# Kernel tuning notes

Hardware: AMD Instinct MI355X
Metric: run time of the kernel (lower is better)

## Reference

```python
import jax, jax.numpy as jnp
import numpy as np
import math

D_K = 64
DROP_P = 0.5

def setup_inputs() -> dict:
    key = jax.random.key(0)
    kq, kk, kv, km = jax.random.split(key, 4)
    B, S, d = 32, 2048, D_K
    Q = jax.random.normal(kq, (B, S, d), dtype=jnp.float32)
    K = jax.random.normal(kk, (B, S, d), dtype=jnp.float32)
    V = jax.random.normal(kv, (B, S, d), dtype=jnp.float32)
    # Bernoulli(keep_prob) mask for training-mode dropout (p=0.5)
    dropout_mask = jax.random.bernoulli(km, 1.0 - DROP_P, (B, S, S))
    return {"Q": Q, "K": K, "V": V, "dropout_mask": dropout_mask}

def reference(Q, K, V, dropout_mask):
    # attn = softmax(Q K^T / sqrt(d_k)); dropout; y = attn V
    scale = 1.0 / math.sqrt(D_K)
    scores = jnp.einsum('bqd,bkd->bqk', Q, K) * scale   # [B,S,S]
    attn = jax.nn.softmax(scores, axis=-1)
    keep_scale = 1.0 / (1.0 - DROP_P)
    attn = jnp.where(dropout_mask, attn * keep_scale, 0.0)
    y = jnp.einsum('bqk,bkd->bqd', attn, V)             # [B,S,d]
    return (y, attn)
```

## Files before the change

kernel.cpp:

```cpp
#include <hip/hip_runtime.h>
#include <hip/hip_bf16.h>
#include <stdint.h>

#define SQ 2048
#define DK 64
#define NB 32
#define TQ 16
#define EW 2064
#define NTHREADS 512
#define SCL 0.18033688011112042f

typedef __attribute__((ext_vector_type(8))) short short8;
typedef __attribute__((ext_vector_type(4))) float f32x4;
typedef __attribute__((ext_vector_type(4))) unsigned u32x4;
typedef __attribute__((ext_vector_type(2))) unsigned u32x2;

__device__ __forceinline__ unsigned f2bf_u(float x) {
    unsigned u = __builtin_bit_cast(unsigned, x);
    u += 0x7fffu + ((u >> 16) & 1u);
    return u >> 16;
}
__device__ __forceinline__ float bf2f(unsigned h) {
    return __builtin_bit_cast(float, h << 16);
}
__device__ __forceinline__ void split8(const float* p, short8& h, short8& l) {
    f32x4 a = *(const f32x4*)p;
    f32x4 b = *(const f32x4*)(p + 4);
    #pragma unroll
    for (int j = 0; j < 4; ++j) {
        unsigned ua = f2bf_u(a[j]);
        h[j] = (short)ua; l[j] = (short)f2bf_u(a[j] - bf2f(ua));
        unsigned ub = f2bf_u(b[j]);
        h[j + 4] = (short)ub; l[j + 4] = (short)f2bf_u(b[j] - bf2f(ub));
    }
}
__device__ __forceinline__ unsigned pkf16(float a, float b) {
    unsigned short ha = __builtin_bit_cast(unsigned short, (_Float16)a);
    unsigned short hb = __builtin_bit_cast(unsigned short, (_Float16)b);
    return (unsigned)ha | ((unsigned)hb << 16);
}
__device__ __forceinline__ float upk16(unsigned u, int hi) {
    return (float)__builtin_bit_cast(_Float16, (unsigned short)(hi ? (u >> 16) : (u & 0xffffu)));
}

__global__ __launch_bounds__(256) void prep_kernel(
    const float* __restrict__ K, const float* __restrict__ V,
    unsigned short* __restrict__ Khi, unsigned short* __restrict__ Klo,
    unsigned short* __restrict__ Vt)
{
    __shared__ float vtile[64][65];
    const int t  = threadIdx.x;
    const int b  = blockIdx.x >> 5;
    const int s0 = (blockIdx.x & 31) << 6;
    const size_t base = ((size_t)b * SQ + s0) * DK + (size_t)t * 16;

    {
        short8 h0, l0, h1, l1;
        split8(K + base,     h0, l0);
        split8(K + base + 8, h1, l1);
        *(short8*)(Khi + base)     = h0;
        *(short8*)(Khi + base + 8) = h1;
        *(short8*)(Klo + base)     = l0;
        *(short8*)(Klo + base + 8) = l1;
    }
    {
        const int sr = t >> 2, dc = (t & 3) << 4;
        #pragma unroll
        for (int u = 0; u < 16; u += 4) {
            f32x4 v = *(const f32x4*)(V + base + u);
            vtile[sr][dc + u + 0] = v[0];
            vtile[sr][dc + u + 1] = v[1];
            vtile[sr][dc + u + 2] = v[2];
            vtile[sr][dc + u + 3] = v[3];
        }
    }
    __syncthreads();
    #pragma unroll
    for (int rep = 0; rep < 16; ++rep) {
        const int idx = rep * 256 + t;
        const int d = idx >> 6, s = idx & 63;
        Vt[((size_t)b * DK + d) * SQ + s0 + s] = (unsigned short)f2bf_u(vtile[s][d]);
    }
}

__global__ __launch_bounds__(NTHREADS, 4) void sdpa_main(
    const float* __restrict__ Q, const unsigned short* __restrict__ Khi,
    const unsigned short* __restrict__ Klo, const unsigned short* __restrict__ Vt,
    const unsigned* __restrict__ Mk, float* __restrict__ Yout, float* __restrict__ Aout)
{
    __shared__ __align__(16) unsigned short e_lds[TQ][EW];
    __shared__ float yp[4][TQ][16];
    __shared__ float rsum[8][TQ];
    __shared__ float i2s[TQ];

    const int tid  = threadIdx.x;
    const int lane = tid & 63;
    const int wv   = tid >> 6;
    const int m16  = lane & 15;
    const int kq   = lane >> 4;
    const int koff = kq * 8;

    const int b  = blockIdx.x >> 7;
    const int q0 = (blockIdx.x & 127) * TQ;

    const int cr = tid >> 5;
    const int cc = (tid & 31) * 8;
    const int xc = (cr & 7) << 3;
    const size_t crow = ((size_t)b * SQ + q0 + cr) * SQ + cc;

    u32x4 ma0 = __builtin_nontemporal_load((const u32x4*)(Mk + crow));
    u32x4 mb0 = __builtin_nontemporal_load((const u32x4*)(Mk + crow + 4));
    u32x4 ma1 = __builtin_nontemporal_load((const u32x4*)(Mk + crow + 256));
    u32x4 mb1 = __builtin_nontemporal_load((const u32x4*)(Mk + crow + 256 + 4));

    short8 qh[2], ql[2];
    {
        const float* qrow = Q + ((size_t)b * SQ + q0 + m16) * DK;
        split8(qrow + koff,      qh[0], ql[0]);
        split8(qrow + 32 + koff, qh[1], ql[1]);
    }

    float rs = 0.f;
    {
        const size_t krow = ((size_t)b * SQ + wv * 256 + m16) * DK;
        const unsigned short* khp = Khi + krow;
        const unsigned short* klp = Klo + krow;
        const int xw = (m16 & 7) << 3;
        for (int t = 0; t < 16; ++t) {
            const int off = t * 16 * DK;
            f32x4 acc = {0.f, 0.f, 0.f, 0.f};
            #pragma unroll
            for (int c = 0; c < 2; ++c) {
                short8 kh = *(const short8*)(khp + off + c * 32 + koff);
                short8 kl = *(const short8*)(klp + off + c * 32 + koff);
                acc = __builtin_amdgcn_mfma_f32_16x16x32_bf16(kh, qh[c], acc, 0, 0, 0);
                acc = __builtin_amdgcn_mfma_f32_16x16x32_bf16(kh, ql[c], acc, 0, 0, 0);
                acc = __builtin_amdgcn_mfma_f32_16x16x32_bf16(kl, qh[c], acc, 0, 0, 0);
            }
            const float e0 = exp2f(acc[0] * SCL);
            const float e1 = exp2f(acc[1] * SCL);
            const float e2 = exp2f(acc[2] * SCL);
            const float e3 = exp2f(acc[3] * SCL);
            rs += (e0 + e1) + (e2 + e3);
            u32x2 pk;
            pk[0] = pkf16(e0, e1);
            pk[1] = pkf16(e2, e3);
            *(u32x2*)&e_lds[m16][(wv * 256 + t * 16 + kq * 4) ^ xw] = pk;
        }
    }
    rs += __shfl_xor(rs, 16);
    rs += __shfl_xor(rs, 32);
    if (lane < 16) rsum[wv][lane] = rs;
    __syncthreads();
    if (tid < 16) {
        float s = 0.f;
        #pragma unroll
        for (int w = 0; w < 8; ++w) s += rsum[w][tid];
        i2s[tid] = 2.0f / s;
    }
    __syncthreads();

    const float i2 = i2s[cr];

    const int g   = wv >> 1;
    const int par = wv & 1;
    const int xm  = (m16 & 7) << 3;
    const unsigned short* vrow = Vt + ((size_t)b * DK + g * 16 + m16) * SQ;
    f32x4 acc = {0.f, 0.f, 0.f, 0.f};

    #define C_FINISH(s, ma, mb)                                                   \
    {                                                                             \
        unsigned short* ep = &e_lds[cr][((s) * 256 + cc) ^ xc];                   \
        const u32x4 ev = *(const u32x4*)ep;                                       \
        const float a0 = (ma)[0] ? upk16(ev[0], 0) * i2 : 0.f;                    \
        const float a1 = (ma)[1] ? upk16(ev[0], 1) * i2 : 0.f;                    \
        const float a2 = (ma)[2] ? upk16(ev[1], 0) * i2 : 0.f;                    \
        const float a3 = (ma)[3] ? upk16(ev[1], 1) * i2 : 0.f;                    \
        const float a4 = (mb)[0] ? upk16(ev[2], 0) * i2 : 0.f;                    \
        const float a5 = (mb)[1] ? upk16(ev[2], 1) * i2 : 0.f;                    \
        const float a6 = (mb)[2] ? upk16(ev[3], 0) * i2 : 0.f;                    \
        const float a7 = (mb)[3] ? upk16(ev[3], 1) * i2 : 0.f;                    \
        f32x4 av0 = {a0, a1, a2, a3};                                             \
        f32x4 av1 = {a4, a5, a6, a7};                                             \
        __builtin_nontemporal_store(av0, (f32x4*)(Aout + crow + (s) * 256));      \
        __builtin_nontemporal_store(av1, (f32x4*)(Aout + crow + (s) * 256 + 4));  \
        u32x4 pb;                                                                 \
        pb[0] = f2bf_u(a0) | (f2bf_u(a1) << 16);                                  \
        pb[1] = f2bf_u(a2) | (f2bf_u(a3) << 16);                                  \
        pb[2] = f2bf_u(a4) | (f2bf_u(a5) << 16);                                  \
        pb[3] = f2bf_u(a6) | (f2bf_u(a7) << 16);                                  \
        *(u32x4*)ep = pb;                                                         \
    }

    #define PV_STRIPE(s)                                                          \
    {                                                                             \
        _Pragma("unroll")                                                         \
        for (int c = 0; c < 4; ++c) {                                             \
            const int k0 = (s) * 256 + par * 128 + c * 32;                        \
            short8 af = *(const short8*)&e_lds[m16][(k0 + koff) ^ xm];            \
            short8 vf = *(const short8*)(vrow + k0 + koff);                       \
            acc = __builtin_amdgcn_mfma_f32_16x16x32_bf16(af, vf, acc, 0, 0, 0);  \
        }                                                                         \
    }

    #define CBAR()                                                                \
        asm volatile("s_waitcnt lgkmcnt(0)" ::: "memory");                        \
        __builtin_amdgcn_s_barrier();                                             \
        __builtin_amdgcn_sched_barrier(0);

    #define REFILL(slotA, slotB, s)                                               \
        slotA = __builtin_nontemporal_load((const u32x4*)(Mk + crow + (s) * 256));\
        slotB = __builtin_nontemporal_load((const u32x4*)(Mk + crow + (s) * 256 + 4));

    C_FINISH(0, ma0, mb0);
    CBAR();

    REFILL(ma0, mb0, 2); PV_STRIPE(0); C_FINISH(1, ma1, mb1); CBAR();
    REFILL(ma1, mb1, 3); PV_STRIPE(1); C_FINISH(2, ma0, mb0); CBAR();
    REFILL(ma0, mb0, 4); PV_STRIPE(2); C_FINISH(3, ma1, mb1); CBAR();
    REFILL(ma1, mb1, 5); PV_STRIPE(3); C_FINISH(4, ma0, mb0); CBAR();
    REFILL(ma0, mb0, 6); PV_STRIPE(4); C_FINISH(5, ma1, mb1); CBAR();
    REFILL(ma1, mb1, 7); PV_STRIPE(5); C_FINISH(6, ma0, mb0); CBAR();
                         PV_STRIPE(6); C_FINISH(7, ma1, mb1); CBAR();
                         PV_STRIPE(7);

    #undef REFILL
    #undef CBAR
    #undef PV_STRIPE
    #undef C_FINISH

    if (par == 1) {
        #pragma unroll
        for (int r = 0; r < 4; ++r) yp[g][kq * 4 + r][m16] = acc[r];
    }
    __syncthreads();
    if (par == 0) {
        #pragma unroll
        for (int r = 0; r < 4; ++r) {
            const float yv = acc[r] + yp[g][kq * 4 + r][m16];
            __builtin_nontemporal_store(yv,
                Yout + ((size_t)b * SQ + q0 + kq * 4 + r) * DK + g * 16 + m16);
        }
    }
}

extern "C" void kernel_launch(void* const* d_in, const int* in_sizes, int n_in,
                              void* d_out, int out_size, void* d_ws, size_t ws_size,
                              hipStream_t stream) {
    const float*    Q  = (const float*)d_in[0];
    const float*    K  = (const float*)d_in[1];
    const float*    V  = (const float*)d_in[2];
    const unsigned* Mk = (const unsigned*)d_in[3];
    float* Yout = (float*)d_out;
    float* Aout = (float*)d_out + (size_t)NB * SQ * DK;

    const size_t NEL = (size_t)NB * SQ * DK;
    unsigned short* Khi = (unsigned short*)d_ws;
    unsigned short* Klo = Khi + NEL;
    unsigned short* Vt  = Klo + NEL;

    prep_kernel<<<dim3(NB * (SQ / 64)), dim3(256), 0, stream>>>(K, V, Khi, Klo, Vt);
    sdpa_main<<<dim3(NB * (SQ / TQ)), dim3(NTHREADS), 0, stream>>>(
        Q, Khi, Klo, Vt, Mk, Yout, Aout);
}
```

Baseline: 499.2 us.

## Apply dropout mask in QK phase and defer normalization to output

Moves the dropout mask application into the QK^T/exp phase, storing masked unnormalized exponentials as bf16 in LDS. The PV matmul now consumes these directly without a per-stripe rewrite pass or barriers, and the 1/sum scale is applied once to Y at the end and to A when it is written. This removes the LDS read-modify-write and the barrier chain between the C and PV stripes. In exchange, attention output values are now rounded to bf16 before scaling, which loses precision compared with the previous fp16 path, and the mask loads move into the compute loop.

```diff
diff --git a/kernel.cpp b/kernel.cpp
--- a/kernel.cpp
+++ b/kernel.cpp
@@ -22,6 +22,9 @@
 }
 __device__ __forceinline__ float bf2f(unsigned h) {
     return __builtin_bit_cast(float, h << 16);
+}
+__device__ __forceinline__ float bf2f_hi(unsigned u) {
+    return __builtin_bit_cast(float, u & 0xffff0000u);
 }
 __device__ __forceinline__ void split8(const float* p, short8& h, short8& l) {
     f32x4 a = *(const f32x4*)p;
@@ -33,14 +36,6 @@
         unsigned ub = f2bf_u(b[j]);
         h[j + 4] = (short)ub; l[j + 4] = (short)f2bf_u(b[j] - bf2f(ub));
     }
-}
-__device__ __forceinline__ unsigned pkf16(float a, float b) {
-    unsigned short ha = __builtin_bit_cast(unsigned short, (_Float16)a);
-    unsigned short hb = __builtin_bit_cast(unsigned short, (_Float16)b);
-    return (unsigned)ha | ((unsigned)hb << 16);
-}
-__device__ __forceinline__ float upk16(unsigned u, int hi) {
-    return (float)__builtin_bit_cast(_Float16, (unsigned short)(hi ? (u >> 16) : (u & 0xffffu)));
 }
 
 __global__ __launch_bounds__(256) void prep_kernel(
@@ -103,64 +98,80 @@
     const int b  = blockIdx.x >> 7;
     const int q0 = (blockIdx.x & 127) * TQ;
 
+    short8 qh[2], ql[2];
+    {
+        const float* qrow = Q + ((size_t)b * SQ + q0 + m16) * DK;
+        split8(qrow + koff,      qh[0], ql[0]);
+        split8(qrow + 32 + koff, qh[1], ql[1]);
+    }
+
+    float rs = 0.f;
+    {
+        const size_t krow = ((size_t)b * SQ + wv * 256 + m16) * DK;
+        const unsigned short* khp = Khi + krow;
+        const unsigned short* klp = Klo + krow;
+        const unsigned* mrow = Mk + ((size_t)b * SQ + q0 + m16) * SQ + wv * 256 + kq * 4;
+        const int xw = (m16 & 7) << 3;
+
+        u32x4 m0, m1, m2, m3, m4, m5, m6, m7;
+
+        #define LOADM(dst, t) dst = *(const u32x4*)(mrow + (t) * 16);
+        #define AITER(t, M)                                                           \
+        {                                                                             \
+            const int off = (t) * 16 * DK;                                            \
+            f32x4 acc = {0.f, 0.f, 0.f, 0.f};                                         \
+            _Pragma("unroll")                                                         \
+            for (int c = 0; c < 2; ++c) {                                             \
+                short8 kh = *(const short8*)(khp + off + c * 32 + koff);              \
+                short8 kl = *(const short8*)(klp + off + c * 32 + koff);              \
+                acc = __builtin_amdgcn_mfma_f32_16x16x32_bf16(kh, qh[c], acc, 0, 0, 0);\
+                acc = __builtin_amdgcn_mfma_f32_16x16x32_bf16(kh, ql[c], acc, 0, 0, 0);\
+                acc = __builtin_amdgcn_mfma_f32_16x16x32_bf16(kl, qh[c], acc, 0, 0, 0);\
+            }                                                                         \
+            const float e0 = exp2f(acc[0] * SCL);                                     \
+            const float e1 = exp2f(acc[1] * SCL);                                     \
+            const float e2 = exp2f(acc[2] * SCL);                                     \
+            const float e3 = exp2f(acc[3] * SCL);                                     \
+            rs += (e0 + e1) + (e2 + e3);                                              \
+            const float a0 = (M)[0] ? e0 : 0.f;                                       \
+            const float a1 = (M)[1] ? e1 : 0.f;                                       \
+            const float a2 = (M)[2] ? e2 : 0.f;                                       \
+            const float a3 = (M)[3] ? e3 : 0.f;                                       \
+            u32x2 pk;                                                                 \
+            pk[0] = f2bf_u(a0) | (f2bf_u(a1) << 16);                                  \
+            pk[1] = f2bf_u(a2) | (f2bf_u(a3) << 16);                                  \
+            *(u32x2*)&e_lds[m16][(wv * 256 + (t) * 16 + kq * 4) ^ xw] = pk;           \
+        }
+
+        LOADM(m0, 0)  LOADM(m1, 1)  LOADM(m2, 2)  LOADM(m3, 3)
+        LOADM(m4, 4)  LOADM(m5, 5)  LOADM(m6, 6)  LOADM(m7, 7)
+        AITER(0, m0)  AITER(1, m1)  AITER(2, m2)  AITER(3, m3)
+        LOADM(m0, 8)  LOADM(m1, 9)  LOADM(m2, 10) LOADM(m3, 11)
+        AITER(4, m4)  AITER(5, m5)  AITER(6, m6)  AITER(7, m7)
+        LOADM(m4, 12) LOADM(m5, 13) LOADM(m6, 14) LOADM(m7, 15)
+        AITER(8, m0)  AITER(9, m1)  AITER(10, m2) AITER(11, m3)
+        AITER(12, m4) AITER(13, m5) AITER(14, m6) AITER(15, m7)
+
+        #undef AITER
+        #undef LOADM
+    }
+    rs += __shfl_xor(rs, 16);
+    rs += __shfl_xor(rs, 32);
+    if (lane < 16) rsum[wv][lane] = rs;
+    __syncthreads();
+    if (tid < 16) {
+        float s = 0.f;
+        #pragma unroll
+        for (int w = 0; w < 8; ++w) s += rsum[w][tid];
+        i2s[tid] = 2.0f / s;
+    }
+    __syncthreads();
+
     const int cr = tid >> 5;
     const int cc = (tid & 31) * 8;
     const int xc = (cr & 7) << 3;
+    const float i2 = i2s[cr];
     const size_t crow = ((size_t)b * SQ + q0 + cr) * SQ + cc;
-
-    u32x4 ma0 = __builtin_nontemporal_load((const u32x4*)(Mk + crow));
-    u32x4 mb0 = __builtin_nontemporal_load((const u32x4*)(Mk + crow + 4));
-    u32x4 ma1 = __builtin_nontemporal_load((const u32x4*)(Mk + crow + 256));
-    u32x4 mb1 = __builtin_nontemporal_load((const u32x4*)(Mk + crow + 256 + 4));
-
-    short8 qh[2], ql[2];
-    {
-        const float* qrow = Q + ((size_t)b * SQ + q0 + m16) * DK;
-        split8(qrow + koff,      qh[0], ql[0]);
-        split8(qrow + 32 + koff, qh[1], ql[1]);
-    }
-
-    float rs = 0.f;
-    {
-        const size_t krow = ((size_t)b * SQ + wv * 256 + m16) * DK;
-        const unsigned short* khp = Khi + krow;
-        const unsigned short* klp = Klo + krow;
-        const int xw = (m16 & 7) << 3;
-        for (int t = 0; t < 16; ++t) {
-            const int off = t * 16 * DK;
-            f32x4 acc = {0.f, 0.f, 0.f, 0.f};
-            #pragma unroll
-            for (int c = 0; c < 2; ++c) {
-                short8 kh = *(const short8*)(khp + off + c * 32 + koff);
-                short8 kl = *(const short8*)(klp + off + c * 32 + koff);
-                acc = __builtin_amdgcn_mfma_f32_16x16x32_bf16(kh, qh[c], acc, 0, 0, 0);
-                acc = __builtin_amdgcn_mfma_f32_16x16x32_bf16(kh, ql[c], acc, 0, 0, 0);
-                acc = __builtin_amdgcn_mfma_f32_16x16x32_bf16(kl, qh[c], acc, 0, 0, 0);
-            }
-            const float e0 = exp2f(acc[0] * SCL);
-            const float e1 = exp2f(acc[1] * SCL);
-            const float e2 = exp2f(acc[2] * SCL);
-            const float e3 = exp2f(acc[3] * SCL);
-            rs += (e0 + e1) + (e2 + e3);
-            u32x2 pk;
-            pk[0] = pkf16(e0, e1);
-            pk[1] = pkf16(e2, e3);
-            *(u32x2*)&e_lds[m16][(wv * 256 + t * 16 + kq * 4) ^ xw] = pk;
-        }
-    }
-    rs += __shfl_xor(rs, 16);
-    rs += __shfl_xor(rs, 32);
-    if (lane < 16) rsum[wv][lane] = rs;
-    __syncthreads();
-    if (tid < 16) {
-        float s = 0.f;
-        #pragma unroll
-        for (int w = 0; w < 8; ++w) s += rsum[w][tid];
-        i2s[tid] = 2.0f / s;
-    }
-    __syncthreads();
-
-    const float i2 = i2s[cr];
 
     const int g   = wv >> 1;
     const int par = wv & 1;
@@ -168,31 +179,18 @@
     const unsigned short* vrow = Vt + ((size_t)b * DK + g * 16 + m16) * SQ;
     f32x4 acc = {0.f, 0.f, 0.f, 0.f};
 
-    #define C_FINISH(s, ma, mb)                                                   \
+    #define CSTRIPE(s)                                                            \
     {                                                                             \
-        unsigned short* ep = &e_lds[cr][((s) * 256 + cc) ^ xc];                   \
-        const u32x4 ev = *(const u32x4*)ep;                                       \
-        const float a0 = (ma)[0] ? upk16(ev[0], 0) * i2 : 0.f;                    \
-        const float a1 = (ma)[1] ? upk16(ev[0], 1) * i2 : 0.f;                    \
-        const float a2 = (ma)[2] ? upk16(ev[1], 0) * i2 : 0.f;                    \
-        const float a3 = (ma)[3] ? upk16(ev[1], 1) * i2 : 0.f;                    \
-        const float a4 = (mb)[0] ? upk16(ev[2], 0) * i2 : 0.f;                    \
-        const float a5 = (mb)[1] ? upk16(ev[2], 1) * i2 : 0.f;                    \
-        const float a6 = (mb)[2] ? upk16(ev[3], 0) * i2 : 0.f;                    \
-        const float a7 = (mb)[3] ? upk16(ev[3], 1) * i2 : 0.f;                    \
-        f32x4 av0 = {a0, a1, a2, a3};                                             \
-        f32x4 av1 = {a4, a5, a6, a7};                                             \
-        __builtin_nontemporal_store(av0, (f32x4*)(Aout + crow + (s) * 256));      \
-        __builtin_nontemporal_store(av1, (f32x4*)(Aout + crow + (s) * 256 + 4));  \
-        u32x4 pb;                                                                 \
-        pb[0] = f2bf_u(a0) | (f2bf_u(a1) << 16);                                  \
-        pb[1] = f2bf_u(a2) | (f2bf_u(a3) << 16);                                  \
-        pb[2] = f2bf_u(a4) | (f2bf_u(a5) << 16);                                  \
-        pb[3] = f2bf_u(a6) | (f2bf_u(a7) << 16);                                  \
-        *(u32x4*)ep = pb;                                                         \
-    }
-
-    #define PV_STRIPE(s)                                                          \
+        const u32x4 ev = *(const u32x4*)&e_lds[cr][((s) * 256 + cc) ^ xc];        \
+        f32x4 o0, o1;                                                             \
+        o0[0] = bf2f(ev[0] & 0xffffu) * i2;  o0[1] = bf2f_hi(ev[0]) * i2;         \
+        o0[2] = bf2f(ev[1] & 0xffffu) * i2;  o0[3] = bf2f_hi(ev[1]) * i2;         \
+        o1[0] = bf2f(ev[2] & 0xffffu) * i2;  o1[1] = bf2f_hi(ev[2]) * i2;         \
+        o1[2] = bf2f(ev[3] & 0xffffu) * i2;  o1[3] = bf2f_hi(ev[3]) * i2;         \
+        __builtin_nontemporal_store(o0, (f32x4*)(Aout + crow + (s) * 256));       \
+        __builtin_nontemporal_store(o1, (f32x4*)(Aout + crow + (s) * 256 + 4));   \
+    }
+    #define PVSTRIPE(s)                                                           \
     {                                                                             \
         _Pragma("unroll")                                                         \
         for (int c = 0; c < 4; ++c) {                                             \
@@ -203,31 +201,17 @@
         }                                                                         \
     }
 
-    #define CBAR()                                                                \
-        asm volatile("s_waitcnt lgkmcnt(0)" ::: "memory");                        \
-        __builtin_amdgcn_s_barrier();                                             \
-        __builtin_amdgcn_sched_barrier(0);
-
-    #define REFILL(slotA, slotB, s)                                               \
-        slotA = __builtin_nontemporal_load((const u32x4*)(Mk + crow + (s) * 256));\
-        slotB = __builtin_nontemporal_load((const u32x4*)(Mk + crow + (s) * 256 + 4));
-
-    C_FINISH(0, ma0, mb0);
-    CBAR();
-
-    REFILL(ma0, mb0, 2); PV_STRIPE(0); C_FINISH(1, ma1, mb1); CBAR();
-    REFILL(ma1, mb1, 3); PV_STRIPE(1); C_FINISH(2, ma0, mb0); CBAR();
-    REFILL(ma0, mb0, 4); PV_STRIPE(2); C_FINISH(3, ma1, mb1); CBAR();
-    REFILL(ma1, mb1, 5); PV_STRIPE(3); C_FINISH(4, ma0, mb0); CBAR();
-    REFILL(ma0, mb0, 6); PV_STRIPE(4); C_FINISH(5, ma1, mb1); CBAR();
-    REFILL(ma1, mb1, 7); PV_STRIPE(5); C_FINISH(6, ma0, mb0); CBAR();
-                         PV_STRIPE(6); C_FINISH(7, ma1, mb1); CBAR();
-                         PV_STRIPE(7);
-
-    #undef REFILL
-    #undef CBAR
-    #undef PV_STRIPE
-    #undef C_FINISH
+    CSTRIPE(0) PVSTRIPE(0)
+    CSTRIPE(1) PVSTRIPE(1)
+    CSTRIPE(2) PVSTRIPE(2)
+    CSTRIPE(3) PVSTRIPE(3)
+    CSTRIPE(4) PVSTRIPE(4)
+    CSTRIPE(5) PVSTRIPE(5)
+    CSTRIPE(6) PVSTRIPE(6)
+    CSTRIPE(7) PVSTRIPE(7)
+
+    #undef PVSTRIPE
+    #undef CSTRIPE
 
     if (par == 1) {
         #pragma unroll
@@ -237,7 +221,7 @@
     if (par == 0) {
         #pragma unroll
         for (int r = 0; r < 4; ++r) {
-            const float yv = acc[r] + yp[g][kq * 4 + r][m16];
+            const float yv = (acc[r] + yp[g][kq * 4 + r][m16]) * i2s[kq * 4 + r];
             __builtin_nontemporal_store(yv,
                 Yout + ((size_t)b * SQ + q0 + kq * 4 + r) * DK + g * 16 + m16);
         }
```

Result: slower. 512.0 us (+2.6%).
